# Kernel tuning notes

Measured on AMD Instinct MI355X. Metric: run time of the kernel, lower is better.

Reference implementation:

```python
import jax, jax.numpy as jnp
import numpy as np

N_NODES = 100000
N_EDGES = 1600000
IN_DIM = 128
HID_DIM = 32
OUT_DIM = 64
N_REL = 8
N_CLASSES = 2


def setup_inputs() -> dict:
    key = jax.random.key(0)
    ks = jax.random.split(key, 12)
    x = jax.random.normal(ks[0], (N_NODES, IN_DIM), dtype=jnp.float32)
    edge_index = jax.random.randint(ks[1], (2, N_EDGES), 0, N_NODES, dtype=jnp.int64)
    edge_type = jax.random.randint(ks[2], (N_EDGES,), 0, N_REL, dtype=jnp.int64)
    # FastRGCNConv params: per-relation weight W [R, in, out], root weight, bias
    def glorot(k, shape):
        fan_in, fan_out = shape[-2], shape[-1]
        s = jnp.sqrt(6.0 / (fan_in + fan_out))
        return jax.random.uniform(k, shape, jnp.float32, -s, s)
    W1 = glorot(ks[3], (N_REL, IN_DIM, HID_DIM))
    root1 = glorot(ks[4], (IN_DIM, HID_DIM))
    b1 = jnp.zeros((HID_DIM,), jnp.float32)
    W2 = glorot(ks[5], (N_REL, HID_DIM, OUT_DIM))
    root2 = glorot(ks[6], (HID_DIM, OUT_DIM))
    b2 = jnp.zeros((OUT_DIM,), jnp.float32)
    lin_w = glorot(ks[7], (OUT_DIM, N_CLASSES))
    lin_b = jnp.zeros((N_CLASSES,), jnp.float32)
    return {"x": x, "edge_index": edge_index, "edge_type": edge_type,
            "W1": W1, "root1": root1, "b1": b1,
            "W2": W2, "root2": root2, "b2": b2,
            "lin_w": lin_w, "lin_b": lin_b}


def _fast_rgcn_conv(x, W, root, b, src, dst, etype, n_nodes):
    """FastRGCNConv: per-relation transform, gather by (src, relation),
    mean-aggregate by destination, plus root transform and bias."""
    # Transform all nodes by all relation weights: [N, R, H]
    xW = jnp.einsum('nf,rfh->nrh', x, W)
    # Per-edge message: relation-specific transformed source feature [E, H]
    msg = xW[src, etype]
    agg = jax.ops.segment_sum(msg, dst, num_segments=n_nodes)
    deg = jax.ops.segment_sum(jnp.ones((src.shape[0],), x.dtype), dst,
                              num_segments=n_nodes)
    agg = agg / jnp.maximum(deg, 1.0)[:, None]  # mean aggregation
    return agg + x @ root + b


def reference(x, edge_index, edge_type, W1, root1, b1, W2, root2, b2, lin_w, lin_b):
    src, dst = edge_index[0], edge_index[1]
    n = x.shape[0]
    h = jax.nn.relu(_fast_rgcn_conv(x, W1, root1, b1, src, dst, edge_type, n))
    h = _fast_rgcn_conv(h, W2, root2, b2, src, dst, edge_type, n)
    return h @ lin_w + lin_b
```

## Files before the change

### kernel.cpp

```cpp
#include <hip/hip_runtime.h>

#define NN      100000
#define IN_DIM  128
#define HID     32
#define ODIM    64
#define L1C     288
#define L2K     288
#define NWGS    196
#define NCB     784
#define CCAP    40
#define RECCAP  2304
#define G2ST    296
#define PST     40
#define HST     40
#define PKCAP   512

using bf16x8 = __attribute__((ext_vector_type(8))) short;
using f32x4  = __attribute__((ext_vector_type(4))) float;

__device__ __forceinline__ float bf2f(short s) {
    unsigned int u = ((unsigned int)(unsigned short)s) << 16;
    float f; __builtin_memcpy(&f, &u, 4); return f;
}
__device__ __forceinline__ short f2bf(float f) {
    unsigned int u; __builtin_memcpy(&u, &f, 4);
    u += 0x7fffu + ((u >> 16) & 1u);
    return (short)(u >> 16);
}
__device__ __forceinline__ float ldf(const void* p, int i, int f32) {
    return f32 ? ((const float*)p)[i] : bf2f(((const short*)p)[i]);
}
__device__ __forceinline__ int ldi(const int* p, long long i, int i64) {
    return i64 ? p[2 * i] : p[(int)i];
}

__global__ __launch_bounds__(1024) void detect(const short* __restrict__ x,
                                               const short* __restrict__ W1,
                                               const short* __restrict__ r1,
                                               const short* __restrict__ W2,
                                               const short* __restrict__ r2,
                                               const short* __restrict__ lw,
                                               const int* __restrict__ ei,
                                               const int* __restrict__ et,
                                               int* __restrict__ flags) {
    __shared__ int cnt[8];
    if (threadIdx.x < 8) cnt[threadIdx.x] = 0;
    __syncthreads();
    const short* ptrs[6] = {x, W1, r1, W2, r2, lw};
    const int    nsmp[6] = {1024, 1024, 1024, 1024, 1024, 64};
    int t = threadIdx.x;
#pragma unroll
    for (int j = 0; j < 6; ++j) {
        if (t < nsmp[j]) {
            unsigned int s = (unsigned short)ptrs[j][2 * t];
            unsigned int e = (s >> 7) & 0xFF;
            if (e >= 140u || (e >= 1u && e <= 100u)) atomicAdd(&cnt[j], 1);
        }
    }
    if (t < 128) {
        if (ei[2 * t + 1] != 0) atomicAdd(&cnt[6], 1);
        if (et[2 * t + 1] != 0) atomicAdd(&cnt[7], 1);
    }
    __syncthreads();
    if (t == 0) {
        const int ns[6] = {1024, 1024, 1024, 1024, 1024, 64};
        for (int j = 0; j < 6; ++j) flags[j] = (cnt[j] * 4 > ns[j]) ? 1 : 0;
        flags[6] = (cnt[6] == 0) ? 1 : 0;
        flags[7] = (cnt[7] == 0) ? 1 : 0;
    }
}

__global__ __launch_bounds__(256) void prep_all(const void* __restrict__ W1,
                                                const void* __restrict__ root1,
                                                const void* __restrict__ W2,
                                                const void* __restrict__ root2,
                                                const short* __restrict__ b1,
                                                const short* __restrict__ b2,
                                                const void* __restrict__ lin_w,
                                                const short* __restrict__ lin_b,
                                                short* __restrict__ w1t,
                                                short* __restrict__ w2ct,
                                                short* __restrict__ smallc,
                                                const int* __restrict__ flags) {
    int gi = blockIdx.x * 256 + threadIdx.x;
    if (gi < L1C * IN_DIM) {
        int c = gi >> 7, f = gi & 127;
        float v;
        if (c < 256) { int r = c >> 5, h = c & 31; v = ldf(W1, (r * IN_DIM + f) * HID + h, flags[1]); }
        else         { v = ldf(root1, f * HID + (c - 256), flags[2]); }
        w1t[c * IN_DIM + f] = f2bf(v);
        return;
    }
    int i2 = gi - L1C * IN_DIM;
    if (i2 < ODIM * L2K) {
        int c = i2 / L2K, k = i2 % L2K;
        float v;
        if (k < 256) { int r = k >> 5, kk = k & 31; v = ldf(W2, (r * HID + kk) * ODIM + c, flags[3]); }
        else         { v = ldf(root2, (k - 256) * ODIM + c, flags[4]); }
        w2ct[c * L2K + k] = f2bf(v);
        return;
    }
    int i3 = i2 - ODIM * L2K;
    if (i3 < 256) {
        if (i3 < 32)        smallc[i3] = b1[i3];
        else if (i3 < 96)   smallc[i3] = b2[i3 - 32];
        else if (i3 < 224)  smallc[i3] = f2bf(ldf(lin_w, i3 - 96, flags[5]));
        else if (i3 < 226)  smallc[i3] = lin_b[i3 - 224];
    }
}

__global__ __launch_bounds__(1024) void scatter_coarse(const int* __restrict__ ei,
                                                       const int* __restrict__ et,
                                                       int* __restrict__ cnt,
                                                       int* __restrict__ seg, int E,
                                                       const int* __restrict__ flags) {
    __shared__ int cur[NCB];
    if (threadIdx.x < NCB) cur[threadIdx.x] = 0;
    __syncthreads();
    int i64 = flags[6], t64 = flags[7];
    int epw = (E + NWGS - 1) / NWGS;
    int lo = blockIdx.x * epw;
    int hi = lo + epw; if (hi > E) hi = E;
    for (int i = lo + threadIdx.x; i < hi; i += 1024) {
        int s = ldi(ei, i, i64);
        int d = ldi(ei, (long long)E + i, i64);
        int r = ldi(et, i, t64);
        int cb = d >> 7;
        int pos = atomicAdd(&cur[cb], 1);
        if (pos < CCAP)
            seg[(cb * NWGS + (int)blockIdx.x) * CCAP + pos] = ((d & 127) << 20) | (s << 3) | r;
    }
    __syncthreads();
    if (threadIdx.x < NCB) {
        int c = cur[threadIdx.x];
        cnt[blockIdx.x * NCB + threadIdx.x] = c < CCAP ? c : CCAP;
    }
}

__global__ __launch_bounds__(64) void cb_sum(const int* __restrict__ cnt,
                                             int* __restrict__ cbTot) {
    int cb = blockIdx.x, lane = threadIdx.x;
    int t = 0;
    for (int g = lane; g < NWGS; g += 64) t += cnt[g * NCB + cb];
#pragma unroll
    for (int o = 32; o > 0; o >>= 1) t += __shfl_down(t, o, 64);
    if (lane == 0) cbTot[cb] = t;
}

__global__ __launch_bounds__(256) void build_cb(const int* __restrict__ cnt,
                                                const int* __restrict__ seg,
                                                const int* __restrict__ cbTot,
                                                int* __restrict__ off,
                                                float* __restrict__ inv_deg,
                                                int* __restrict__ packed) {
    __shared__ int cntl[NWGS], soff[NWGS];
    __shared__ int recs[RECCAP];
    __shared__ int degl[128], basel[128], kcur[128];
    __shared__ int stmp[256];
    __shared__ int gbase_s;
    int cb = blockIdx.x, tid = threadIdx.x;
    {
        int part = 0;
        for (int j = tid; j < cb; j += 256) part += cbTot[j];
        stmp[tid] = part; __syncthreads();
        for (int o = 128; o > 0; o >>= 1) {
            if (tid < o) stmp[tid] += stmp[tid + o];
            __syncthreads();
        }
        if (tid == 0) gbase_s = stmp[0];
        __syncthreads();
    }
    if (tid < NWGS) cntl[tid] = cnt[tid * NCB + cb];
    if (tid < 128) degl[tid] = 0;
    __syncthreads();
    int v = (tid < NWGS) ? cntl[tid] : 0;
    stmp[tid] = v; __syncthreads();
    for (int o = 1; o < 256; o <<= 1) {
        int u = (tid >= o) ? stmp[tid - o] : 0;
        __syncthreads();
        stmp[tid] += u;
        __syncthreads();
    }
    if (tid < NWGS) soff[tid] = stmp[tid] - v;
    int tot = stmp[255]; if (tot > RECCAP) tot = RECCAP;
    __syncthreads();
    int wave = tid >> 6, lane = tid & 63;
    for (int g = wave; g < NWGS; g += 4) {
        int c = cntl[g], b = soff[g];
        const int* sp = seg + (cb * NWGS + g) * CCAP;
        for (int e = lane; e < c; e += 64)
            if (b + e < RECCAP) recs[b + e] = sp[e];
    }
    __syncthreads();
    for (int i = tid; i < tot; i += 256) atomicAdd(&degl[recs[i] >> 20], 1);
    __syncthreads();
    int dv = (tid < 128) ? degl[tid] : 0;
    stmp[tid] = dv; __syncthreads();
    for (int o = 1; o < 128; o <<= 1) {
        int u = (tid >= o) ? stmp[tid - o] : 0;
        __syncthreads();
        stmp[tid] += u;
        __syncthreads();
    }
    int gbase = gbase_s;
    if (tid < 128) {
        int excl = stmp[tid] - dv;
        basel[tid] = excl;
        kcur[tid] = 0;
        int node = cb * 128 + tid;
        if (node <= NN) {
            off[node] = gbase + excl;
            if (node < NN) inv_deg[node] = 1.0f / (float)(dv > 1 ? dv : 1);
        }
    }
    __syncthreads();
    for (int i = tid; i < tot; i += 256) {
        int rec = recs[i];
        int n = rec >> 20;
        int p = atomicAdd(&kcur[n], 1);
        packed[gbase + basel[n] + p] = ((n & 15) << 24) | (rec & 0xFFFFF);
    }
}

__global__ __launch_bounds__(256) void gemm1(const void* __restrict__ x,
                                             const short* __restrict__ w1t,
                                             short* __restrict__ xw,
                                             const int* __restrict__ flags) {
    int wave = threadIdx.x >> 6, lane = threadIdx.x & 63;
    int m = lane & 15, quad = lane >> 4;
    int row0 = (blockIdx.x * 4 + wave) * 64;
    if (row0 >= NN) return;

    bf16x8 a[4][4];
    int fp32 = flags[0];
#pragma unroll
    for (int t = 0; t < 4; ++t) {
        int row = row0 + t * 16 + m;
        int rc = row < NN ? row : NN - 1;
        if (fp32) {
            const float* xr = (const float*)x + rc * IN_DIM + quad * 8;
#pragma unroll
            for (int kt = 0; kt < 4; ++kt) {
                const f32x4* q = (const f32x4*)(xr + kt * 32);
                f32x4 u0 = q[0], u1 = q[1];
                bf16x8 tt;
                tt[0] = f2bf(u0[0]); tt[1] = f2bf(u0[1]); tt[2] = f2bf(u0[2]); tt[3] = f2bf(u0[3]);
                tt[4] = f2bf(u1[0]); tt[5] = f2bf(u1[1]); tt[6] = f2bf(u1[2]); tt[7] = f2bf(u1[3]);
                a[t][kt] = tt;
            }
        } else {
            const short* xr = (const short*)x + rc * IN_DIM + quad * 8;
#pragma unroll
            for (int kt = 0; kt < 4; ++kt) a[t][kt] = *(const bf16x8*)(xr + kt * 32);
        }
    }

    for (int ct = 0; ct < 18; ++ct) {
        const short* wp = w1t + (ct * 16 + m) * IN_DIM + quad * 8;
        bf16x8 b[4];
#pragma unroll
        for (int kt = 0; kt < 4; ++kt) b[kt] = *(const bf16x8*)(wp + kt * 32);
#pragma unroll
        for (int t = 0; t < 4; ++t) {
            f32x4 acc = {0.f, 0.f, 0.f, 0.f};
#pragma unroll
            for (int kt = 0; kt < 4; ++kt)
                acc = __builtin_amdgcn_mfma_f32_16x16x32_bf16(a[t][kt], b[kt], acc, 0, 0, 0);
#pragma unroll
            for (int i = 0; i < 4; ++i) {
                int r = row0 + t * 16 + quad * 4 + i;
                if (r < NN) xw[r * L1C + ct * 16 + m] = f2bf(acc[i]);
            }
        }
    }
}

__global__ __launch_bounds__(256) void agg1(const short* __restrict__ xw,
                                            const int* __restrict__ off,
                                            const int* __restrict__ packed,
                                            const float* __restrict__ inv_deg,
                                            const short* __restrict__ smallc,
                                            short* __restrict__ h) {
    int lane = threadIdx.x & 31;
    int node = blockIdx.x * 8 + (threadIdx.x >> 5);
    if (node >= NN) return;
    int s = off[node], e = off[node + 1];
    float acc = 0.f;
    int i = s;
    for (; i + 7 < e; i += 8) {
        int pk0 = packed[i],     pk1 = packed[i + 1], pk2 = packed[i + 2], pk3 = packed[i + 3];
        int pk4 = packed[i + 4], pk5 = packed[i + 5], pk6 = packed[i + 6], pk7 = packed[i + 7];
        float v0 = bf2f(xw[((pk0 >> 3) & 0x1FFFF) * L1C + (pk0 & 7) * 32 + lane]);
        float v1 = bf2f(xw[((pk1 >> 3) & 0x1FFFF) * L1C + (pk1 & 7) * 32 + lane]);
        float v2 = bf2f(xw[((pk2 >> 3) & 0x1FFFF) * L1C + (pk2 & 7) * 32 + lane]);
        float v3 = bf2f(xw[((pk3 >> 3) & 0x1FFFF) * L1C + (pk3 & 7) * 32 + lane]);
        float v4 = bf2f(xw[((pk4 >> 3) & 0x1FFFF) * L1C + (pk4 & 7) * 32 + lane]);
        float v5 = bf2f(xw[((pk5 >> 3) & 0x1FFFF) * L1C + (pk5 & 7) * 32 + lane]);
        float v6 = bf2f(xw[((pk6 >> 3) & 0x1FFFF) * L1C + (pk6 & 7) * 32 + lane]);
        float v7 = bf2f(xw[((pk7 >> 3) & 0x1FFFF) * L1C + (pk7 & 7) * 32 + lane]);
        acc += ((v0 + v1) + (v2 + v3)) + ((v4 + v5) + (v6 + v7));
    }
    for (; i + 3 < e; i += 4) {
        int pk0 = packed[i], pk1 = packed[i + 1], pk2 = packed[i + 2], pk3 = packed[i + 3];
        float v0 = bf2f(xw[((pk0 >> 3) & 0x1FFFF) * L1C + (pk0 & 7) * 32 + lane]);
        float v1 = bf2f(xw[((pk1 >> 3) & 0x1FFFF) * L1C + (pk1 & 7) * 32 + lane]);
        float v2 = bf2f(xw[((pk2 >> 3) & 0x1FFFF) * L1C + (pk2 & 7) * 32 + lane]);
        float v3 = bf2f(xw[((pk3 >> 3) & 0x1FFFF) * L1C + (pk3 & 7) * 32 + lane]);
        acc += (v0 + v1) + (v2 + v3);
    }
    for (; i < e; ++i) {
        int pk = packed[i];
        acc += bf2f(xw[((pk >> 3) & 0x1FFFF) * L1C + (pk & 7) * 32 + lane]);
    }
    float v = acc * inv_deg[node] + bf2f(xw[node * L1C + 256 + lane]) + bf2f(smallc[lane]);
    h[node * HID + lane] = f2bf(v > 0.f ? v : 0.f);
}

__global__ __launch_bounds__(256) void agg2_fused(const short* __restrict__ h,
                                                  const int* __restrict__ off,
                                                  const int* __restrict__ packed,
                                                  const float* __restrict__ inv_deg,
                                                  const short* __restrict__ w2ct,
                                                  const short* __restrict__ smallc,
                                                  float* __restrict__ out) {
    __shared__ __align__(16) short Pl[128 * PST];
    __shared__ __align__(16) short HgT[32 * HST];
    __shared__ int pk_l[PKCAP];
    __shared__ float red[4][16][2];
    __shared__ float invl[16];
    short* g2l = &Pl[0];
    int tid = threadIdx.x;
    int row0 = blockIdx.x * 16;
    if (tid < 16) invl[tid] = inv_deg[row0 + tid];
    int st = off[row0], en = off[row0 + 16];
    int tot = en - st;

    int wave = tid >> 6, lane = tid & 63;
    int m15 = lane & 15, quad = lane >> 4;
    int e = tid & 31;
    int part = tid >> 5;

    {
        uint4 z = {0, 0, 0, 0};
        uint4* pz = (uint4*)&Pl[0];
#pragma unroll
        for (int j = 0; j < 3; ++j) {
            int ix = tid + j * 256;
            if (ix < 640) pz[ix] = z;
        }
        for (int j = tid; j < tot && j < PKCAP; j += 256) pk_l[j] = packed[st + j];
    }
    __syncthreads();

    f32x4 acc00 = {0,0,0,0}, acc01 = {0,0,0,0}, acc10 = {0,0,0,0}, acc11 = {0,0,0,0};
    int prevrow = -1;
    int nchunk = (tot + 31) >> 5;

    int pk = (e < tot) ? ((e < PKCAP) ? pk_l[e] : packed[st + e]) : 0;
    uint2 hv = *(const uint2*)(h + ((pk >> 3) & 0x1FFFF) * HID + part * 4);

    for (int c = 0; c < nchunk; ++c) {
        int valid = (c * 32 + e) < tot;
        if (tid < 32 && prevrow >= 0) Pl[prevrow * PST + e] = 0;
        HgT[(part * 4 + 0) * HST + e] = (short)(hv.x & 0xFFFF);
        HgT[(part * 4 + 1) * HST + e] = (short)(hv.x >> 16);
        HgT[(part * 4 + 2) * HST + e] = (short)(hv.y & 0xFFFF);
        HgT[(part * 4 + 3) * HST + e] = (short)(hv.y >> 16);
        if (tid < 32) {
            if (valid) {
                int row = ((pk >> 24) & 15) * 8 + (pk & 7);
                Pl[row * PST + e] = (short)0x3F80;
                prevrow = row;
            } else prevrow = -1;
        }
        int idx = (c + 1) * 32 + e;
        int pkn = (idx < tot) ? ((idx < PKCAP) ? pk_l[idx] : packed[st + idx]) : 0;
        uint2 hvn = *(const uint2*)(h + ((pkn >> 3) & 0x1FFFF) * HID + part * 4);
        __syncthreads();
        bf16x8 a0 = *(const bf16x8*)(&HgT[m15 * HST + quad * 8]);
        bf16x8 a1 = *(const bf16x8*)(&HgT[(m15 + 16) * HST + quad * 8]);
        bf16x8 b0 = *(const bf16x8*)(&Pl[((wave * 2 + 0) * 16 + m15) * PST + quad * 8]);
        bf16x8 b1 = *(const bf16x8*)(&Pl[((wave * 2 + 1) * 16 + m15) * PST + quad * 8]);
        acc00 = __builtin_amdgcn_mfma_f32_16x16x32_bf16(a0, b0, acc00, 0, 0, 0);
        acc10 = __builtin_amdgcn_mfma_f32_16x16x32_bf16(a1, b0, acc10, 0, 0, 0);
        acc01 = __builtin_amdgcn_mfma_f32_16x16x32_bf16(a0, b1, acc01, 0, 0, 0);
        acc11 = __builtin_amdgcn_mfma_f32_16x16x32_bf16(a1, b1, acc11, 0, 0, 0);
        __syncthreads();
        pk = pkn; hv = hvn;
    }

    {
        int nr0 = (wave * 2 + 0) * 16 + m15;
        int nr1 = (wave * 2 + 1) * 16 + m15;
        float sc0 = invl[nr0 >> 3], sc1 = invl[nr1 >> 3];
        int d0 = quad * 4;
#pragma unroll
        for (int i = 0; i < 4; ++i) {
            g2l[(nr0 >> 3) * G2ST + (nr0 & 7) * 32 + d0 + i]      = f2bf(acc00[i] * sc0);
            g2l[(nr0 >> 3) * G2ST + (nr0 & 7) * 32 + 16 + d0 + i] = f2bf(acc10[i] * sc0);
            g2l[(nr1 >> 3) * G2ST + (nr1 & 7) * 32 + d0 + i]      = f2bf(acc01[i] * sc1);
            g2l[(nr1 >> 3) * G2ST + (nr1 & 7) * 32 + 16 + d0 + i] = f2bf(acc11[i] * sc1);
        }
    }
    for (int j = tid; j < 16 * 32; j += 256) {
        int node = j >> 5, d = j & 31;
        g2l[node * G2ST + 256 + d] = h[(row0 + node) * HID + d];
    }
    __syncthreads();

    const short* wp = w2ct + (wave * 16 + m15) * L2K + quad * 8;
    bf16x8 a[9], b[9];
#pragma unroll
    for (int kt = 0; kt < 9; ++kt) {
        b[kt] = *(const bf16x8*)(wp + kt * 32);
        a[kt] = *(const bf16x8*)(&g2l[m15 * G2ST + quad * 8 + kt * 32]);
    }
    f32x4 acc = {0.f, 0.f, 0.f, 0.f};
#pragma unroll
    for (int kt = 0; kt < 9; ++kt)
        acc = __builtin_amdgcn_mfma_f32_16x16x32_bf16(a[kt], b[kt], acc, 0, 0, 0);

    int c = wave * 16 + m15;
    float lw0 = bf2f(smallc[96 + c * 2 + 0]);
    float lw1 = bf2f(smallc[96 + c * 2 + 1]);
    float b2c = bf2f(smallc[32 + c]);
    float pr0[4], pr1[4];
#pragma unroll
    for (int i = 0; i < 4; ++i) {
        float v = acc[i] + b2c;
        pr0[i] = v * lw0;
        pr1[i] = v * lw1;
    }
#pragma unroll
    for (int o = 1; o < 16; o <<= 1) {
#pragma unroll
        for (int i = 0; i < 4; ++i) {
            pr0[i] += __shfl_xor(pr0[i], o, 64);
            pr1[i] += __shfl_xor(pr1[i], o, 64);
        }
    }
    if (m15 == 0) {
#pragma unroll
        for (int i = 0; i < 4; ++i) {
            red[wave][quad * 4 + i][0] = pr0[i];
            red[wave][quad * 4 + i][1] = pr1[i];
        }
    }
    __syncthreads();
    if (tid < 32) {
        int row = tid >> 1, j = tid & 1;
        float v = red[0][row][j] + red[1][row][j] + red[2][row][j] + red[3][row][j]
                + bf2f(smallc[224 + j]);
        out[(row0 + row) * 2 + j] = v;
    }
}

extern "C" void kernel_launch(void* const* d_in, const int* in_sizes, int n_in,
                              void* d_out, int out_size, void* d_ws, size_t ws_size,
                              hipStream_t stream) {
    const void* x     = d_in[0];
    const int*  ei    = (const int*)d_in[1];
    const int*  etype = (const int*)d_in[2];
    const void* W1    = d_in[3];
    const void* root1 = d_in[4];
    const void* b1    = d_in[5];
    const void* W2    = d_in[6];
    const void* root2 = d_in[7];
    const void* b2    = d_in[8];
    const void* lin_w = d_in[9];
    const void* lin_b = d_in[10];
    float* out = (float*)d_out;

    const int E = in_sizes[2];

    char* p = (char*)d_ws;
    auto alloc = [&](size_t bytes) { char* r = p; p += (bytes + 255) & ~(size_t)255; return (void*)r; };
    int*   flags   = (int*)  alloc(256);
    int*   off     = (int*)  alloc((size_t)(NN + 1) * 4);
    float* inv_deg = (float*)alloc((size_t)NN * 4);
    int*   packed  = (int*)  alloc((size_t)E * 4);
    int*   cnt     = (int*)  alloc((size_t)NWGS * NCB * 4);
    int*   cbTot   = (int*)  alloc((size_t)NCB * 4);
    int*   seg     = (int*)  alloc((size_t)NCB * NWGS * CCAP * 4);
    short* w1t     = (short*)alloc((size_t)L1C * IN_DIM * 2);
    short* w2ct    = (short*)alloc((size_t)ODIM * L2K * 2);
    short* smallc  = (short*)alloc(256 * 2);
    short* h       = (short*)alloc((size_t)NN * HID * 2);
    short* xw1     = (short*)alloc((size_t)NN * L1C * 2);

    detect<<<1, 1024, 0, stream>>>((const short*)x, (const short*)W1, (const short*)root1,
                                   (const short*)W2, (const short*)root2, (const short*)lin_w,
                                   ei, etype, flags);
    const int prep_items = L1C * IN_DIM + ODIM * L2K + 256;
    prep_all<<<(prep_items + 255) / 256, 256, 0, stream>>>(W1, root1, W2, root2,
                                                           (const short*)b1, (const short*)b2,
                                                           lin_w, (const short*)lin_b,
                                                           w1t, w2ct, smallc, flags);

    scatter_coarse<<<NWGS, 1024, 0, stream>>>(ei, etype, cnt, seg, E, flags);
    cb_sum<<<NCB, 64, 0, stream>>>(cnt, cbTot);
    build_cb<<<NCB, 256, 0, stream>>>(cnt, seg, cbTot, off, inv_deg, packed);

    gemm1<<<((NN + 63) / 64 + 3) / 4, 256, 0, stream>>>(x, w1t, xw1, flags);
    agg1<<<(NN + 7) / 8, 256, 0, stream>>>(xw1, off, packed, inv_deg, smallc, h);
    agg2_fused<<<NN / 16, 256, 0, stream>>>(h, off, packed, inv_deg, w2ct, smallc, out);
}
```

Before: 300.4 us.

## Sort edges by (node, relation) and replace MFMA scatter-matmul with segmented sums

The CSR build now buckets each node's edges by relation, using an 8x finer degree histogram and prefix scan, so each node's packed edge list is grouped by relation. Layer-2 aggregation drops the MFMA one-hot matrix trick, which staged gathered h rows and an indicator matrix in LDS with two barriers per 32-edge chunk. Instead each node gets 16 threads that run a segmented sum over relation runs and write per-relation means directly into the G2 tile. This removes barriers and most of the padded matrix work, but it brings divergent per-thread loops whose cost depends on degree imbalance, and 4-byte gathers per thread instead of wider vector loads.

```diff
diff --git a/kernel.cpp b/kernel.cpp
--- a/kernel.cpp
+++ b/kernel.cpp
@@ -11,9 +11,6 @@
 #define CCAP    40
 #define RECCAP  2304
 #define G2ST    296
-#define PST     40
-#define HST     40
-#define PKCAP   512
 
 using bf16x8 = __attribute__((ext_vector_type(8))) short;
 using f32x4  = __attribute__((ext_vector_type(4))) float;
@@ -155,7 +152,7 @@
                                                 int* __restrict__ packed) {
     __shared__ int cntl[NWGS], soff[NWGS];
     __shared__ int recs[RECCAP];
-    __shared__ int degl[128], basel[128], kcur[128];
+    __shared__ int deg8[1024], base8[1024], kcur8[1024];
     __shared__ int stmp[256];
     __shared__ int gbase_s;
     int cb = blockIdx.x, tid = threadIdx.x;
@@ -171,7 +168,8 @@
         __syncthreads();
     }
     if (tid < NWGS) cntl[tid] = cnt[tid * NCB + cb];
-    if (tid < 128) degl[tid] = 0;
+#pragma unroll
+    for (int j = 0; j < 4; ++j) { deg8[tid + j * 256] = 0; kcur8[tid + j * 256] = 0; }
     __syncthreads();
     int v = (tid < NWGS) ? cntl[tid] : 0;
     stmp[tid] = v; __syncthreads();
@@ -192,33 +190,42 @@
             if (b + e < RECCAP) recs[b + e] = sp[e];
     }
     __syncthreads();
-    for (int i = tid; i < tot; i += 256) atomicAdd(&degl[recs[i] >> 20], 1);
-    __syncthreads();
-    int dv = (tid < 128) ? degl[tid] : 0;
-    stmp[tid] = dv; __syncthreads();
-    for (int o = 1; o < 128; o <<= 1) {
+    for (int i = tid; i < tot; i += 256) {
+        int rec = recs[i];
+        atomicAdd(&deg8[((rec >> 20) << 3) | (rec & 7)], 1);
+    }
+    __syncthreads();
+    int k0 = tid * 4;
+    int d0 = deg8[k0], d1 = deg8[k0 + 1], d2 = deg8[k0 + 2], d3 = deg8[k0 + 3];
+    int s01 = d0 + d1, sum4 = s01 + d2 + d3;
+    stmp[tid] = sum4; __syncthreads();
+    for (int o = 1; o < 256; o <<= 1) {
         int u = (tid >= o) ? stmp[tid - o] : 0;
         __syncthreads();
         stmp[tid] += u;
         __syncthreads();
     }
+    int excl = stmp[tid] - sum4;
+    base8[k0] = excl; base8[k0 + 1] = excl + d0;
+    base8[k0 + 2] = excl + s01; base8[k0 + 3] = excl + s01 + d2;
+    __syncthreads();
     int gbase = gbase_s;
     if (tid < 128) {
-        int excl = stmp[tid] - dv;
-        basel[tid] = excl;
-        kcur[tid] = 0;
+        int b0 = base8[tid * 8];
+        int b1 = (tid < 127) ? base8[(tid + 1) * 8] : tot;
+        int dv = b1 - b0;
         int node = cb * 128 + tid;
         if (node <= NN) {
-            off[node] = gbase + excl;
+            off[node] = gbase + b0;
             if (node < NN) inv_deg[node] = 1.0f / (float)(dv > 1 ? dv : 1);
         }
     }
     __syncthreads();
     for (int i = tid; i < tot; i += 256) {
         int rec = recs[i];
-        int n = rec >> 20;
-        int p = atomicAdd(&kcur[n], 1);
-        packed[gbase + basel[n] + p] = ((n & 15) << 24) | (rec & 0xFFFFF);
+        int key = ((rec >> 20) << 3) | (rec & 7);
+        int p = atomicAdd(&kcur8[key], 1);
+        packed[gbase + base8[key] + p] = (((rec >> 20) & 15) << 24) | (rec & 0xFFFFF);
     }
 }
 
@@ -323,91 +330,65 @@
                                                   const short* __restrict__ w2ct,
                                                   const short* __restrict__ smallc,
                                                   float* __restrict__ out) {
-    __shared__ __align__(16) short Pl[128 * PST];
-    __shared__ __align__(16) short HgT[32 * HST];
-    __shared__ int pk_l[PKCAP];
+    __shared__ __align__(16) short g2l[16 * G2ST];
     __shared__ float red[4][16][2];
     __shared__ float invl[16];
-    short* g2l = &Pl[0];
     int tid = threadIdx.x;
     int row0 = blockIdx.x * 16;
     if (tid < 16) invl[tid] = inv_deg[row0 + tid];
-    int st = off[row0], en = off[row0 + 16];
-    int tot = en - st;
+    {
+        unsigned* gz = (unsigned*)g2l;
+        const int nu = 16 * G2ST / 2;
+        for (int j = tid; j < nu; j += 256) gz[j] = 0;
+    }
+    __syncthreads();
+
+    int node = tid >> 4, l = tid & 15;
+    int st = off[row0 + node], en = off[row0 + node + 1];
+    float inv = invl[node];
+    const short* hp = h + l * 2;
+    short* grow = g2l + node * G2ST + l * 2;
+    float a0 = 0.f, a1 = 0.f;
+    int cur = -1;
+
+    auto acc_edge = [&](int pk, unsigned hv) {
+        int rel = pk & 7;
+        if (rel != cur) {
+            if (cur >= 0) {
+                unsigned w = ((unsigned)(unsigned short)f2bf(a1 * inv) << 16)
+                           | (unsigned short)f2bf(a0 * inv);
+                *(unsigned*)(grow + cur * 32) = w;
+            }
+            a0 = 0.f; a1 = 0.f; cur = rel;
+        }
+        a0 += bf2f((short)(hv & 0xFFFF));
+        a1 += bf2f((short)(hv >> 16));
+    };
+
+    int i = st;
+    for (; i + 3 < en; i += 4) {
+        int p0 = packed[i], p1 = packed[i + 1], p2 = packed[i + 2], p3 = packed[i + 3];
+        unsigned v0 = *(const unsigned*)(hp + ((p0 >> 3) & 0x1FFFF) * HID);
+        unsigned v1 = *(const unsigned*)(hp + ((p1 >> 3) & 0x1FFFF) * HID);
+        unsigned v2 = *(const unsigned*)(hp + ((p2 >> 3) & 0x1FFFF) * HID);
+        unsigned v3 = *(const unsigned*)(hp + ((p3 >> 3) & 0x1FFFF) * HID);
+        acc_edge(p0, v0); acc_edge(p1, v1); acc_edge(p2, v2); acc_edge(p3, v3);
+    }
+    for (; i < en; ++i) {
+        int p = packed[i];
+        unsigned v = *(const unsigned*)(hp + ((p >> 3) & 0x1FFFF) * HID);
+        acc_edge(p, v);
+    }
+    if (cur >= 0) {
+        unsigned w = ((unsigned)(unsigned short)f2bf(a1 * inv) << 16)
+                   | (unsigned short)f2bf(a0 * inv);
+        *(unsigned*)(grow + cur * 32) = w;
+    }
+    *(unsigned*)(grow + 256) = *(const unsigned*)(h + (row0 + node) * HID + l * 2);
+    __syncthreads();
 
     int wave = tid >> 6, lane = tid & 63;
     int m15 = lane & 15, quad = lane >> 4;
-    int e = tid & 31;
-    int part = tid >> 5;
-
-    {
-        uint4 z = {0, 0, 0, 0};
-        uint4* pz = (uint4*)&Pl[0];
-#pragma unroll
-        for (int j = 0; j < 3; ++j) {
-            int ix = tid + j * 256;
-            if (ix < 640) pz[ix] = z;
-        }
-        for (int j = tid; j < tot && j < PKCAP; j += 256) pk_l[j] = packed[st + j];
-    }
-    __syncthreads();
-
-    f32x4 acc00 = {0,0,0,0}, acc01 = {0,0,0,0}, acc10 = {0,0,0,0}, acc11 = {0,0,0,0};
-    int prevrow = -1;
-    int nchunk = (tot + 31) >> 5;
-
-    int pk = (e < tot) ? ((e < PKCAP) ? pk_l[e] : packed[st + e]) : 0;
-    uint2 hv = *(const uint2*)(h + ((pk >> 3) & 0x1FFFF) * HID + part * 4);
-
-    for (int c = 0; c < nchunk; ++c) {
-        int valid = (c * 32 + e) < tot;
-        if (tid < 32 && prevrow >= 0) Pl[prevrow * PST + e] = 0;
-        HgT[(part * 4 + 0) * HST + e] = (short)(hv.x & 0xFFFF);
-        HgT[(part * 4 + 1) * HST + e] = (short)(hv.x >> 16);
-        HgT[(part * 4 + 2) * HST + e] = (short)(hv.y & 0xFFFF);
-        HgT[(part * 4 + 3) * HST + e] = (short)(hv.y >> 16);
-        if (tid < 32) {
-            if (valid) {
-                int row = ((pk >> 24) & 15) * 8 + (pk & 7);
-                Pl[row * PST + e] = (short)0x3F80;
-                prevrow = row;
-            } else prevrow = -1;
-        }
-        int idx = (c + 1) * 32 + e;
-        int pkn = (idx < tot) ? ((idx < PKCAP) ? pk_l[idx] : packed[st + idx]) : 0;
-        uint2 hvn = *(const uint2*)(h + ((pkn >> 3) & 0x1FFFF) * HID + part * 4);
-        __syncthreads();
-        bf16x8 a0 = *(const bf16x8*)(&HgT[m15 * HST + quad * 8]);
-        bf16x8 a1 = *(const bf16x8*)(&HgT[(m15 + 16) * HST + quad * 8]);
-        bf16x8 b0 = *(const bf16x8*)(&Pl[((wave * 2 + 0) * 16 + m15) * PST + quad * 8]);
-        bf16x8 b1 = *(const bf16x8*)(&Pl[((wave * 2 + 1) * 16 + m15) * PST + quad * 8]);
-        acc00 = __builtin_amdgcn_mfma_f32_16x16x32_bf16(a0, b0, acc00, 0, 0, 0);
-        acc10 = __builtin_amdgcn_mfma_f32_16x16x32_bf16(a1, b0, acc10, 0, 0, 0);
-        acc01 = __builtin_amdgcn_mfma_f32_16x16x32_bf16(a0, b1, acc01, 0, 0, 0);
-        acc11 = __builtin_amdgcn_mfma_f32_16x16x32_bf16(a1, b1, acc11, 0, 0, 0);
-        __syncthreads();
-        pk = pkn; hv = hvn;
-    }
-
-    {
-        int nr0 = (wave * 2 + 0) * 16 + m15;
-        int nr1 = (wave * 2 + 1) * 16 + m15;
-        float sc0 = invl[nr0 >> 3], sc1 = invl[nr1 >> 3];
-        int d0 = quad * 4;
-#pragma unroll
-        for (int i = 0; i < 4; ++i) {
-            g2l[(nr0 >> 3) * G2ST + (nr0 & 7) * 32 + d0 + i]      = f2bf(acc00[i] * sc0);
-            g2l[(nr0 >> 3) * G2ST + (nr0 & 7) * 32 + 16 + d0 + i] = f2bf(acc10[i] * sc0);
-            g2l[(nr1 >> 3) * G2ST + (nr1 & 7) * 32 + d0 + i]      = f2bf(acc01[i] * sc1);
-            g2l[(nr1 >> 3) * G2ST + (nr1 & 7) * 32 + 16 + d0 + i] = f2bf(acc11[i] * sc1);
-        }
-    }
-    for (int j = tid; j < 16 * 32; j += 256) {
-        int node = j >> 5, d = j & 31;
-        g2l[node * G2ST + 256 + d] = h[(row0 + node) * HID + d];
-    }
-    __syncthreads();
-
     const short* wp = w2ct + (wave * 16 + m15) * L2K + quad * 8;
     bf16x8 a[9], b[9];
 #pragma unroll
@@ -426,24 +407,24 @@
     float b2c = bf2f(smallc[32 + c]);
     float pr0[4], pr1[4];
 #pragma unroll
-    for (int i = 0; i < 4; ++i) {
-        float v = acc[i] + b2c;
-        pr0[i] = v * lw0;
-        pr1[i] = v * lw1;
+    for (int i2 = 0; i2 < 4; ++i2) {
+        float v = acc[i2] + b2c;
+        pr0[i2] = v * lw0;
+        pr1[i2] = v * lw1;
     }
 #pragma unroll
     for (int o = 1; o < 16; o <<= 1) {
 #pragma unroll
-        for (int i = 0; i < 4; ++i) {
-            pr0[i] += __shfl_xor(pr0[i], o, 64);
-            pr1[i] += __shfl_xor(pr1[i], o, 64);
+        for (int i2 = 0; i2 < 4; ++i2) {
+            pr0[i2] += __shfl_xor(pr0[i2], o, 64);
+            pr1[i2] += __shfl_xor(pr1[i2], o, 64);
         }
     }
     if (m15 == 0) {
 #pragma unroll
-        for (int i = 0; i < 4; ++i) {
-            red[wave][quad * 4 + i][0] = pr0[i];
-            red[wave][quad * 4 + i][1] = pr1[i];
+        for (int i2 = 0; i2 < 4; ++i2) {
+            red[wave][quad * 4 + i2][0] = pr0[i2];
+            red[wave][quad * 4 + i2][1] = pr1[i2];
         }
     }
     __syncthreads();
```

Measured after the change: 288.8 us. 1.04x faster.
